# Kernel tuning notes

Hardware: AMD Instinct MI355X
Metric: run time of the kernel (lower is better)

The kernel has to match this reference:

```python
import jax, jax.numpy as jnp
import numpy as np

DEPTH = 2
DIM = 192
HEADS = 6
MLP_RATIO = 4

def _layernorm(x, g, b):
    mu = jnp.mean(x, -1, keepdims=True)
    var = jnp.var(x, -1, keepdims=True)
    return (x - mu) * jax.lax.rsqrt(var + 1e-5) * g + b

def _scanline_order(pos, w):
    # default space-filling curve of space_filling_cluster: horizontal scanlines
    # with alternating direction in each row (boustrophedon order)
    ix = jnp.floor(pos[..., 0]).astype(jnp.int32)
    iy = jnp.floor(pos[..., 1]).astype(jnp.int32)
    key = iy * w + jnp.where(iy % 2 == 1, w - 1 - ix, ix)
    order_idx = jnp.argsort(key, axis=1)      # rank -> token idx (b, n)
    inv_idx = jnp.argsort(order_idx, axis=1)  # token idx -> rank (b, n)
    return order_idx, inv_idx

def setup_inputs():
    key = jax.random.key(0)
    ks = jax.random.split(key, 8)
    b, h, w, m = 4, 128, 128, 64
    n = h * w
    d = DIM
    dff = MLP_RATIO * d
    s = 0.02
    x = jax.random.normal(ks[0], (b, n, d), jnp.float32)
    # token positions: the full h x w grid, randomly permuted per batch element
    ys, xs = jnp.meshgrid(jnp.arange(h), jnp.arange(w), indexing='ij')
    grid = jnp.stack([xs.reshape(-1), ys.reshape(-1)], -1).astype(jnp.float32)
    perm = jax.vmap(lambda kk: jax.random.permutation(kk, n))(jax.random.split(ks[1], b))
    pos = grid[perm]  # (b, n, 2)
    return {
        'x': x, 'pos': pos,
        'ln1_g': jnp.ones((DEPTH, d)), 'ln1_b': jnp.zeros((DEPTH, d)),
        'w_qkv': jax.random.normal(ks[2], (DEPTH, d, 3 * d), jnp.float32) * s,
        'b_qkv': jnp.zeros((DEPTH, 3 * d)),
        'w_proj': jax.random.normal(ks[3], (DEPTH, d, d), jnp.float32) * s,
        'b_proj': jnp.zeros((DEPTH, d)),
        'ln2_g': jnp.ones((DEPTH, d)), 'ln2_b': jnp.zeros((DEPTH, d)),
        'w_fc1': jax.random.normal(ks[4], (DEPTH, d, dff), jnp.float32) * s,
        'b_fc1': jnp.zeros((DEPTH, dff)),
        'w_fc2': jax.random.normal(ks[5], (DEPTH, dff, d), jnp.float32) * s,
        'b_fc2': jnp.zeros((DEPTH, d)),
        'h': h, 'w': w, 'm': m,
    }

def reference(x, pos, ln1_g, ln1_b, w_qkv, b_qkv, w_proj, b_proj,
              ln2_g, ln2_b, w_fc1, b_fc1, w_fc2, b_fc2, h, w, m):
    b, n, d = x.shape
    dh = d // HEADS
    scale = dh ** -0.5
    kc = n // m  # number of clusters (n chosen divisible by m -> all-ones cluster_mask)
    # clustering is computed under no_grad in the original -> stop_gradient
    order_idx, inv_idx = _scanline_order(jax.lax.stop_gradient(pos), w)
    for i in range(DEPTH):
        # --- cluster attention ---
        xn = _layernorm(x, ln1_g[i], ln1_b[i])
        qkv = xn @ w_qkv[i] + b_qkv[i]                                  # (b, n, 3d)
        qkv = jnp.take_along_axis(qkv, order_idx[..., None], axis=1)    # gather into curve order
        qkv = qkv.reshape(b, kc, m, 3, HEADS, dh)
        q = jnp.transpose(qkv[:, :, :, 0], (0, 1, 3, 2, 4))             # (b, kc, H, m, dh)
        kk = jnp.transpose(qkv[:, :, :, 1], (0, 1, 3, 2, 4))
        v = jnp.transpose(qkv[:, :, :, 2], (0, 1, 3, 2, 4))
        att = jax.nn.softmax(jnp.einsum('bkhqd,bkhpd->bkhqp', q, kk) * scale, axis=-1)
        o = jnp.einsum('bkhqp,bkhpd->bkhqd', att, v)
        o = jnp.transpose(o, (0, 1, 3, 2, 4)).reshape(b, n, d)
        o = jnp.take_along_axis(o, inv_idx[..., None], axis=1)          # scatter back to token order
        x = x + o @ w_proj[i] + b_proj[i]
        # --- MLP ---
        yn = _layernorm(x, ln2_g[i], ln2_b[i])
        x = x + jax.nn.gelu(yn @ w_fc1[i] + b_fc1[i]) @ w_fc2[i] + b_fc2[i]
    return x
```

## Files before the change

kernel.cpp:

```cpp
#include <hip/hip_runtime.h>
#include <hip/hip_bf16.h>

typedef __hip_bfloat16 bf16;
typedef __attribute__((ext_vector_type(8))) short short8;
typedef __attribute__((ext_vector_type(4))) short s16x4;
typedef __attribute__((ext_vector_type(4))) float f32x4;

#define B_   4
#define N_   16384
#define D_   192
#define H6   6
#define DH   32
#define MCL  64
#define KC   256
#define DFF  768
#define GW   128
#define MTOK (B_ * N_)
#define XST  196
#define PST  72
#define OST  40

__device__ __forceinline__ bf16 f2b(float x) { return __float2bfloat16(x); }
__device__ __forceinline__ short f2bbits(float x) {
    bf16 h = __float2bfloat16(x); return *(short*)&h;
}

__global__ void zero_out_kernel(float* __restrict__ out, size_t n) {
    size_t i = blockIdx.x * (size_t)blockDim.x + threadIdx.x;
    if (i < n) out[i] = 0.f;
}

__global__ void build_idx(const float* __restrict__ pos, int* __restrict__ order) {
    int tid = blockIdx.x * blockDim.x + threadIdx.x;
    if (tid >= B_ * N_) return;
    int b = tid / N_;
    int ix = (int)floorf(pos[(size_t)tid * 2 + 0]);
    int iy = (int)floorf(pos[(size_t)tid * 2 + 1]);
    int key = iy * GW + ((iy & 1) ? (GW - 1 - ix) : ix);
    key = (int)(((unsigned)key) & (N_ - 1));
    order[(size_t)b * N_ + key] = tid % N_;
}

__global__ void wprep_all(const float* __restrict__ wq, const float* __restrict__ wp,
                          const float* __restrict__ wf1, const float* __restrict__ wf2,
                          bf16* __restrict__ out) {
    int tid = blockIdx.x * blockDim.x + threadIdx.x;
    if (tid >= 2 * 442368) return;
    int l = tid / 442368, r = tid % 442368;
    const float* src; bf16* dst; int K, Nn, e;
    if (r < 110592)      { src = wq  + (size_t)l * 110592; dst = out + (size_t)l * 442368;          K = 192; Nn = 576; e = r; }
    else if (r < 147456) { src = wp  + (size_t)l * 36864;  dst = out + (size_t)l * 442368 + 110592; K = 192; Nn = 192; e = r - 110592; }
    else if (r < 294912) { src = wf1 + (size_t)l * 147456; dst = out + (size_t)l * 442368 + 147456; K = 192; Nn = 768; e = r - 147456; }
    else                 { src = wf2 + (size_t)l * 147456; dst = out + (size_t)l * 442368 + 294912; K = 768; Nn = 192; e = r - 294912; }
    int k = e / Nn, n = e % Nn;
    int idx = ((n >> 4) * (K >> 5) + (k >> 5)) * 512 + (((k >> 3) & 3) * 16 + (n & 15)) * 8 + (k & 7);
    dst[idx] = f2b(src[e]);
}

__global__ __launch_bounds__(384) void qa_fused(
    const float* __restrict__ xsrc, const int* __restrict__ order,
    const float* __restrict__ lng, const float* __restrict__ lnb,
    const bf16* __restrict__ Wqf, const float* __restrict__ bq,
    bf16* __restrict__ outb) {
    __shared__ short Asl[4 * 6 * 512];
    __shared__ short Qf[4 * 6 * 512];
    __shared__ short Kf[4 * 6 * 512];
    __shared__ short Vf[6 * 4 * 512];
    __shared__ short Pm[6 * 64 * PST];
    const float scale = 0.17677669529663687f;
    int c = blockIdx.x, b = blockIdx.y;
    int tid = threadIdx.x;
    int w = tid >> 6, lane = tid & 63;
    int quad = lane >> 4, l16 = lane & 15;
    int t = (int)(((unsigned)order[(size_t)b * N_ + c * MCL + lane]) & (N_ - 1));
    if (tid < 256) {
        int r = tid >> 2, qq = tid & 3;
        int tr = (int)(((unsigned)order[(size_t)b * N_ + c * MCL + r]) & (N_ - 1));
        const float* xr = xsrc + ((size_t)b * N_ + tr) * 192 + qq * 48;
        float4 va[12];
        float s = 0.f, ss = 0.f;
        #pragma unroll
        for (int j = 0; j < 12; j++) {
            va[j] = ((const float4*)xr)[j];
            s  += va[j].x + va[j].y + va[j].z + va[j].w;
            ss += va[j].x * va[j].x + va[j].y * va[j].y + va[j].z * va[j].z + va[j].w * va[j].w;
        }
        s  += __shfl_xor(s, 1);  s  += __shfl_xor(s, 2);
        ss += __shfl_xor(ss, 1); ss += __shfl_xor(ss, 2);
        float mean = s * (1.f / 192.f);
        float var  = ss * (1.f / 192.f) - mean * mean;
        float rs   = rsqrtf(var + 1e-5f);
        const float4* gg = (const float4*)(lng + qq * 48);
        const float4* bb = (const float4*)(lnb + qq * 48);
        #pragma unroll
        for (int j = 0; j < 6; j++) {
            float4 g0 = gg[2 * j], g1 = gg[2 * j + 1], b0 = bb[2 * j], b1v = bb[2 * j + 1];
            float4 x0 = va[2 * j], x1 = va[2 * j + 1];
            short8 o;
            o[0] = f2bbits((x0.x - mean) * rs * g0.x + b0.x);
            o[1] = f2bbits((x0.y - mean) * rs * g0.y + b0.y);
            o[2] = f2bbits((x0.z - mean) * rs * g0.z + b0.z);
            o[3] = f2bbits((x0.w - mean) * rs * g0.w + b0.w);
            o[4] = f2bbits((x1.x - mean) * rs * g1.x + b1v.x);
            o[5] = f2bbits((x1.y - mean) * rs * g1.y + b1v.y);
            o[6] = f2bbits((x1.z - mean) * rs * g1.z + b1v.z);
            o[7] = f2bbits((x1.w - mean) * rs * g1.w + b1v.w);
            int k0 = qq * 48 + j * 8;
            int kt = k0 >> 5, qd = (k0 >> 3) & 3;
            *(short8*)&Asl[((r >> 4) * 6 + kt) * 512 + (qd * 16 + (r & 15)) * 8] = o;
        }
    }
    __syncthreads();
    short8 af[4][6];
    #pragma unroll
    for (int mt = 0; mt < 4; mt++)
        #pragma unroll
        for (int kt = 0; kt < 6; kt++)
            af[mt][kt] = *(short8*)&Asl[(mt * 6 + kt) * 512 + lane * 8];
    #pragma unroll
    for (int s = 0; s < 4; s++) {
        int isK = s >> 1, q = s & 1;
        int nt = isK * 12 + 2 * w + q;
        const short* bp = (const short*)Wqf + ((size_t)nt * 6) * 512 + lane * 8;
        short8 bfr[6];
        #pragma unroll
        for (int kt = 0; kt < 6; kt++) bfr[kt] = *(const short8*)(bp + kt * 512);
        float4 bvq = *(const float4*)(bq + nt * 16 + quad * 4);
        short* dstb = isK ? Kf : Qf;
        #pragma unroll
        for (int mt = 0; mt < 4; mt++) {
            f32x4 a = {};
            #pragma unroll
            for (int kt = 0; kt < 6; kt++)
                a = __builtin_amdgcn_mfma_f32_16x16x32_bf16(bfr[kt], af[mt][kt], a, 0, 0, 0);
            s16x4 o;
            o[0] = f2bbits(a[0] + bvq.x); o[1] = f2bbits(a[1] + bvq.y);
            o[2] = f2bbits(a[2] + bvq.z); o[3] = f2bbits(a[3] + bvq.w);
            *(s16x4*)&dstb[(mt * 6 + w) * 512
                           + ((q * 2 + (quad >> 1)) * 16 + l16) * 8 + (quad & 1) * 4] = o;
        }
    }
    #pragma unroll
    for (int q = 0; q < 2; q++) {
        int nt = 24 + 2 * w + q;
        const short* bp = (const short*)Wqf + ((size_t)nt * 6) * 512 + lane * 8;
        short8 bfr[6];
        #pragma unroll
        for (int kt = 0; kt < 6; kt++) bfr[kt] = *(const short8*)(bp + kt * 512);
        float bvv = bq[nt * 16 + l16];
        #pragma unroll
        for (int mt = 0; mt < 4; mt++) {
            f32x4 a = {};
            #pragma unroll
            for (int kt = 0; kt < 6; kt++)
                a = __builtin_amdgcn_mfma_f32_16x16x32_bf16(af[mt][kt], bfr[kt], a, 0, 0, 0);
            s16x4 o;
            #pragma unroll
            for (int rr = 0; rr < 4; rr++) o[rr] = f2bbits(a[rr] + bvv);
            *(s16x4*)&Vf[((w * 2 + q) * 2 + (mt >> 1)) * 512
                         + (((mt & 1) * 2 + (quad >> 1)) * 16 + l16) * 8 + (quad & 1) * 4] = o;
        }
    }
    short8 aq[4], bk[4];
    #pragma unroll
    for (int i = 0; i < 4; i++) {
        aq[i] = *(short8*)&Qf[(i * 6 + w) * 512 + lane * 8];
        bk[i] = *(short8*)&Kf[(i * 6 + w) * 512 + lane * 8];
    }
    f32x4 S[4][4];
    #pragma unroll
    for (int mt = 0; mt < 4; mt++)
        #pragma unroll
        for (int nt = 0; nt < 4; nt++) {
            f32x4 z = {};
            S[mt][nt] = __builtin_amdgcn_mfma_f32_16x16x32_bf16(aq[mt], bk[nt], z, 0, 0, 0);
        }
    short* Pl = Pm + w * 64 * PST;
    #pragma unroll
    for (int mt = 0; mt < 4; mt++)
        #pragma unroll
        for (int r = 0; r < 4; r++) {
            float e0, e1, e2, e3, s;
            float v0 = S[mt][0][r] * scale, v1 = S[mt][1][r] * scale;
            float v2 = S[mt][2][r] * scale, v3 = S[mt][3][r] * scale;
            e0 = __expf(fminf(fmaxf(v0, -30.f), 30.f));
            e1 = __expf(fminf(fmaxf(v1, -30.f), 30.f));
            e2 = __expf(fminf(fmaxf(v2, -30.f), 30.f));
            e3 = __expf(fminf(fmaxf(v3, -30.f), 30.f));
            s = e0 + e1 + e2 + e3;
            s += __shfl_xor(s, 1); s += __shfl_xor(s, 2);
            s += __shfl_xor(s, 4); s += __shfl_xor(s, 8);
            float inv = 1.f / s;
            int row = mt * 16 + quad * 4 + r;
            Pl[row * PST +  0 + l16] = f2bbits(e0 * inv);
            Pl[row * PST + 16 + l16] = f2bbits(e1 * inv);
            Pl[row * PST + 32 + l16] = f2bbits(e2 * inv);
            Pl[row * PST + 48 + l16] = f2bbits(e3 * inv);
        }
    short8 ap[4][2], bv[2][2];
    #pragma unroll
    for (int mt = 0; mt < 4; mt++)
        #pragma unroll
        for (int kt = 0; kt < 2; kt++)
            ap[mt][kt] = *(const short8*)&Pl[(mt * 16 + l16) * PST + kt * 32 + quad * 8];
    #pragma unroll
    for (int nt = 0; nt < 2; nt++)
        #pragma unroll
        for (int kt = 0; kt < 2; kt++)
            bv[nt][kt] = *(const short8*)&Vf[((w * 2 + nt) * 2 + kt) * 512 + lane * 8];
    f32x4 O[4][2] = {};
    #pragma unroll
    for (int mt = 0; mt < 4; mt++)
        #pragma unroll
        for (int nt = 0; nt < 2; nt++)
            #pragma unroll
            for (int kt = 0; kt < 2; kt++)
                O[mt][nt] = __builtin_amdgcn_mfma_f32_16x16x32_bf16(ap[mt][kt], bv[nt][kt], O[mt][nt], 0, 0, 0);
    short* Ol = Pl;
    #pragma unroll
    for (int mt = 0; mt < 4; mt++) {
        int row = mt * 16 + quad * 4;
        #pragma unroll
        for (int nt = 0; nt < 2; nt++)
            #pragma unroll
            for (int rr = 0; rr < 4; rr++)
                Ol[(row + rr) * OST + nt * 16 + l16] = f2bbits(O[mt][nt][rr]);
    }
    short* op = (short*)outb + ((size_t)b * N_ + t) * 192 + w * 32;
    #pragma unroll
    for (int j = 0; j < 4; j++)
        *(short8*)(op + j * 8) = *(const short8*)&Ol[lane * OST + j * 8];
}

__global__ __launch_bounds__(256) void pm_fused(
    const bf16* __restrict__ Anob,
    const bf16* __restrict__ Wpf, const float* __restrict__ bp_,
    const float* __restrict__ Rsrc,
    const float* __restrict__ lng, const float* __restrict__ lnb,
    const bf16* __restrict__ W1f, const float* __restrict__ b1,
    const bf16* __restrict__ W2f, const float* __restrict__ b2,
    float* __restrict__ Rdst) {
    __shared__ float Xl[64 * XST];
    __shared__ short Bsl[4 * 6 * 512];
    short* Asl = (short*)Xl;
    int tid = threadIdx.x;
    int bm = blockIdx.x;
    int w = tid >> 6, lane = tid & 63;
    int quad = lane >> 4, l16 = lane & 15;
    {
        int r = tid >> 2, qq = tid & 3;
        const short* ar = (const short*)Anob + ((size_t)(bm * 64) + r) * 192 + qq * 48;
        #pragma unroll
        for (int j = 0; j < 6; j++) {
            short8 v = *(const short8*)(ar + j * 8);
            int k0 = qq * 48 + j * 8;
            int kt = k0 >> 5, qd = (k0 >> 3) & 3;
            *(short8*)&Asl[((r >> 4) * 6 + kt) * 512 + (qd * 16 + (r & 15)) * 8] = v;
        }
    }
    __syncthreads();
    short8 afp[6];
    #pragma unroll
    for (int kt = 0; kt < 6; kt++)
        afp[kt] = *(short8*)&Asl[(w * 6 + kt) * 512 + lane * 8];
    f32x4 acc[12];
    #pragma unroll
    for (int nt = 0; nt < 12; nt++) {
        const short* bp = (const short*)Wpf + ((size_t)nt * 6) * 512 + lane * 8;
        f32x4 a = {};
        #pragma unroll
        for (int kt = 0; kt < 6; kt++) {
            short8 b = *(const short8*)(bp + kt * 512);
            a = __builtin_amdgcn_mfma_f32_16x16x32_bf16(afp[kt], b, a, 0, 0, 0);
        }
        acc[nt] = a;
    }
    __syncthreads();
    #pragma unroll
    for (int nt = 0; nt < 12; nt++) {
        int col = nt * 16 + l16;
        float bv = bp_[col];
        int lr0 = w * 16 + quad * 4;
        #pragma unroll
        for (int rr = 0; rr < 4; rr++) {
            float rv = Rsrc[(size_t)(bm * 64 + lr0 + rr) * 192 + col];
            Xl[(lr0 + rr) * XST + col] = acc[nt][rr] + bv + rv;
        }
    }
    __syncthreads();
    {
        int r = tid >> 2, qq = tid & 3;
        const float* xr = &Xl[r * XST + qq * 48];
        float4 va[12];
        float s = 0.f, ss = 0.f;
        #pragma unroll
        for (int j = 0; j < 12; j++) {
            va[j] = ((const float4*)xr)[j];
            s  += va[j].x + va[j].y + va[j].z + va[j].w;
            ss += va[j].x * va[j].x + va[j].y * va[j].y + va[j].z * va[j].z + va[j].w * va[j].w;
        }
        s  += __shfl_xor(s, 1);  s  += __shfl_xor(s, 2);
        ss += __shfl_xor(ss, 1); ss += __shfl_xor(ss, 2);
        float mean = s * (1.f / 192.f);
        float var  = ss * (1.f / 192.f) - mean * mean;
        float rs   = rsqrtf(var + 1e-5f);
        const float4* gg = (const float4*)(lng + qq * 48);
        const float4* bb = (const float4*)(lnb + qq * 48);
        #pragma unroll
        for (int j = 0; j < 6; j++) {
            float4 g0 = gg[2 * j], g1 = gg[2 * j + 1], b0 = bb[2 * j], b1v = bb[2 * j + 1];
            float4 x0 = va[2 * j], x1 = va[2 * j + 1];
            short8 o;
            o[0] = f2bbits((x0.x - mean) * rs * g0.x + b0.x);
            o[1] = f2bbits((x0.y - mean) * rs * g0.y + b0.y);
            o[2] = f2bbits((x0.z - mean) * rs * g0.z + b0.z);
            o[3] = f2bbits((x0.w - mean) * rs * g0.w + b0.w);
            o[4] = f2bbits((x1.x - mean) * rs * g1.x + b1v.x);
            o[5] = f2bbits((x1.y - mean) * rs * g1.y + b1v.y);
            o[6] = f2bbits((x1.z - mean) * rs * g1.z + b1v.z);
            o[7] = f2bbits((x1.w - mean) * rs * g1.w + b1v.w);
            int k0 = qq * 48 + j * 8;
            int kt = k0 >> 5, qd = (k0 >> 3) & 3;
            *(short8*)&Bsl[((r >> 4) * 6 + kt) * 512 + (qd * 16 + (r & 15)) * 8] = o;
        }
    }
    __syncthreads();
    short8 af[4][6];
    #pragma unroll
    for (int mt = 0; mt < 4; mt++)
        #pragma unroll
        for (int kt = 0; kt < 6; kt++)
            af[mt][kt] = *(short8*)&Bsl[(mt * 6 + kt) * 512 + lane * 8];
    f32x4 acc2[3][4] = {};
    for (int qtr = 0; qtr < 4; qtr++) {
        __syncthreads();
        #pragma unroll
        for (int j = 0; j < 3; j++) {
            int nth = w * 3 + j;
            int ntg = qtr * 12 + nth;
            const short* bp = (const short*)W1f + ((size_t)ntg * 6) * 512 + lane * 8;
            short8 bfr[6];
            #pragma unroll
            for (int kt = 0; kt < 6; kt++) bfr[kt] = *(const short8*)(bp + kt * 512);
            #pragma unroll
            for (int mt = 0; mt < 4; mt++) {
                f32x4 a = {};
                #pragma unroll
                for (int kt = 0; kt < 6; kt++)
                    a = __builtin_amdgcn_mfma_f32_16x16x32_bf16(bfr[kt], af[mt][kt], a, 0, 0, 0);
                int colb = ntg * 16 + quad * 4;
                s16x4 o;
                #pragma unroll
                for (int rr = 0; rr < 4; rr++) {
                    float u = a[rr] + b1[colb + rr];
                    float inner = 0.7978845608028654f * (u + 0.044715f * u * u * u);
                    inner = fminf(fmaxf(inner, -12.f), 12.f);
                    float e = __expf(2.f * inner);
                    o[rr] = f2bbits(0.5f * u * (1.f + (e - 1.f) / (e + 1.f)));
                }
                *(s16x4*)&Bsl[(mt * 6 + (nth >> 1)) * 512
                              + (((nth & 1) * 2 + (quad >> 1)) * 16 + l16) * 8 + (quad & 1) * 4] = o;
            }
        }
        __syncthreads();
        #pragma unroll
        for (int kt = 0; kt < 6; kt++) {
            short8 afh[4];
            #pragma unroll
            for (int mt = 0; mt < 4; mt++)
                afh[mt] = *(short8*)&Bsl[(mt * 6 + kt) * 512 + lane * 8];
            #pragma unroll
            for (int j = 0; j < 3; j++) {
                int nt = w * 3 + j;
                const short* bp = (const short*)W2f + ((size_t)nt * 24 + qtr * 6 + kt) * 512 + lane * 8;
                short8 b = *(const short8*)bp;
                #pragma unroll
                for (int mt = 0; mt < 4; mt++)
                    acc2[j][mt] = __builtin_amdgcn_mfma_f32_16x16x32_bf16(afh[mt], b, acc2[j][mt], 0, 0, 0);
            }
        }
    }
    #pragma unroll
    for (int j = 0; j < 3; j++) {
        int col = (w * 3 + j) * 16 + l16;
        float bv = b2[col];
        #pragma unroll
        for (int mt = 0; mt < 4; mt++) {
            int lr0 = mt * 16 + quad * 4;
            #pragma unroll
            for (int rr = 0; rr < 4; rr++) {
                size_t idx = (size_t)(bm * 64 + lr0 + rr) * 192 + col;
                Rdst[idx] = acc2[j][mt][rr] + bv + Xl[(lr0 + rr) * XST + col];
            }
        }
    }
}

extern "C" void kernel_launch(void* const* d_in, const int* in_sizes, int n_in,
                              void* d_out, int out_size, void* d_ws, size_t ws_size,
                              hipStream_t stream) {
    const float* x_in   = (const float*)d_in[0];
    const float* pos    = (const float*)d_in[1];
    const float* ln1_g  = (const float*)d_in[2];
    const float* ln1_b  = (const float*)d_in[3];
    const float* w_qkv  = (const float*)d_in[4];
    const float* b_qkv  = (const float*)d_in[5];
    const float* w_proj = (const float*)d_in[6];
    const float* b_proj = (const float*)d_in[7];
    const float* ln2_g  = (const float*)d_in[8];
    const float* ln2_b  = (const float*)d_in[9];
    const float* w_fc1  = (const float*)d_in[10];
    const float* b_fc1  = (const float*)d_in[11];
    const float* w_fc2  = (const float*)d_in[12];
    const float* b_fc2  = (const float*)d_in[13];

    size_t sz_x     = (size_t)MTOK * D_ * 4;
    size_t sz_xnob  = (size_t)MTOK * D_ * 2;
    size_t sz_order = (size_t)B_ * N_ * 4;
    size_t sz_wbuf  = (size_t)2 * 442368 * 2;
    size_t need = sz_x + sz_xnob + sz_order + sz_wbuf;
    if (ws_size < need) {
        zero_out_kernel<<<(out_size + 255) / 256, 256, 0, stream>>>((float*)d_out, (size_t)out_size);
        return;
    }
    char* ws = (char*)d_ws;
    float* x_f32 = (float*)ws;  ws += sz_x;
    bf16*  xnob  = (bf16*)ws;   ws += sz_xnob;
    int*   order = (int*)ws;    ws += sz_order;
    bf16*  wbuf  = (bf16*)ws;   ws += sz_wbuf;

    bf16* wq[2]; bf16* wp[2]; bf16* wf1[2]; bf16* wf2[2];
    for (int l = 0; l < 2; ++l) {
        bf16* p = wbuf + (size_t)l * 442368;
        wq[l]  = p;
        wp[l]  = p + 110592;
        wf1[l] = p + 147456;
        wf2[l] = p + 294912;
    }
    wprep_all<<<(2 * 442368 + 255) / 256, 256, 0, stream>>>(w_qkv, w_proj, w_fc1, w_fc2, wbuf);
    build_idx<<<(B_ * N_ + 255) / 256, 256, 0, stream>>>(pos, order);

    for (int l = 0; l < 2; ++l) {
        const float* xsrc = (l == 0) ? x_in : x_f32;
        float* rdst = (l == 1) ? (float*)d_out : x_f32;
        qa_fused<<<dim3(KC, B_), 384, 0, stream>>>(
            xsrc, order, ln1_g + l * D_, ln1_b + l * D_,
            wq[l], b_qkv + l * 576, xnob);
        pm_fused<<<MTOK / 64, 256, 0, stream>>>(
            xnob, wp[l], b_proj + l * 192, xsrc,
            ln2_g + l * D_, ln2_b + l * D_,
            wf1[l], b_fc1 + l * 768, wf2[l], b_fc2 + l * 192,
            rdst);
    }
}
```

Before: 440.3 us.

## Fuse cluster attention, projection and MLP into one per-layer kernel

Merges the attention kernel and the projection+MLP kernel into a single kernel launched per cluster. The attention output now stays in shared memory and feeds the projection directly, removing the bf16 intermediate buffer's global write and read plus one launch per layer. The residual read and final output write now go to gathered, scattered token rows instead of contiguous rows. The MLP work is spread over six waves instead of four, and shared-memory regions are aliased across phases, which keeps LDS usage at about 150 KB per block.

```diff
diff --git a/kernel.cpp b/kernel.cpp
--- a/kernel.cpp
+++ b/kernel.cpp
@@ -18,7 +18,6 @@
 #define MTOK (B_ * N_)
 #define XST  196
 #define PST  72
-#define OST  40
 
 __device__ __forceinline__ bf16 f2b(float x) { return __float2bfloat16(x); }
 __device__ __forceinline__ short f2bbits(float x) {
@@ -57,16 +56,24 @@
     dst[idx] = f2b(src[e]);
 }
 
-__global__ __launch_bounds__(384) void qa_fused(
+__global__ __launch_bounds__(384) void layer_fused(
     const float* __restrict__ xsrc, const int* __restrict__ order,
-    const float* __restrict__ lng, const float* __restrict__ lnb,
+    const float* __restrict__ ln1g, const float* __restrict__ ln1b,
     const bf16* __restrict__ Wqf, const float* __restrict__ bq,
-    bf16* __restrict__ outb) {
-    __shared__ short Asl[4 * 6 * 512];
-    __shared__ short Qf[4 * 6 * 512];
-    __shared__ short Kf[4 * 6 * 512];
-    __shared__ short Vf[6 * 4 * 512];
-    __shared__ short Pm[6 * 64 * PST];
+    const bf16* __restrict__ Wpf, const float* __restrict__ bp_,
+    const float* __restrict__ ln2g, const float* __restrict__ ln2b,
+    const bf16* __restrict__ W1f, const float* __restrict__ b1,
+    const bf16* __restrict__ W2f, const float* __restrict__ b2,
+    float* __restrict__ Rdst) {
+    __shared__ __align__(16) char smem[153600];
+    short* Asl = (short*)smem;
+    short* Qf  = (short*)(smem + 24576);
+    short* Kf  = (short*)(smem + 49152);
+    short* Vf  = (short*)(smem + 73728);
+    short* Pm  = (short*)(smem + 98304);
+    float* Xl  = (float*)(smem + 98304);
+    short* Of  = Asl;
+    short* Bsl = Qf;
     const float scale = 0.17677669529663687f;
     int c = blockIdx.x, b = blockIdx.y;
     int tid = threadIdx.x;
@@ -90,8 +97,8 @@
         float mean = s * (1.f / 192.f);
         float var  = ss * (1.f / 192.f) - mean * mean;
         float rs   = rsqrtf(var + 1e-5f);
-        const float4* gg = (const float4*)(lng + qq * 48);
-        const float4* bb = (const float4*)(lnb + qq * 48);
+        const float4* gg = (const float4*)(ln1g + qq * 48);
+        const float4* bb = (const float4*)(ln1b + qq * 48);
         #pragma unroll
         for (int j = 0; j < 6; j++) {
             float4 g0 = gg[2 * j], g1 = gg[2 * j + 1], b0 = bb[2 * j], b1v = bb[2 * j + 1];
@@ -117,6 +124,7 @@
         #pragma unroll
         for (int kt = 0; kt < 6; kt++)
             af[mt][kt] = *(short8*)&Asl[(mt * 6 + kt) * 512 + lane * 8];
+    __syncthreads();
     #pragma unroll
     for (int s = 0; s < 4; s++) {
         int isK = s >> 1, q = s & 1;
@@ -161,134 +169,97 @@
                          + (((mt & 1) * 2 + (quad >> 1)) * 16 + l16) * 8 + (quad & 1) * 4] = o;
         }
     }
-    short8 aq[4], bk[4];
-    #pragma unroll
-    for (int i = 0; i < 4; i++) {
-        aq[i] = *(short8*)&Qf[(i * 6 + w) * 512 + lane * 8];
-        bk[i] = *(short8*)&Kf[(i * 6 + w) * 512 + lane * 8];
-    }
-    f32x4 S[4][4];
-    #pragma unroll
-    for (int mt = 0; mt < 4; mt++)
-        #pragma unroll
-        for (int nt = 0; nt < 4; nt++) {
-            f32x4 z = {};
-            S[mt][nt] = __builtin_amdgcn_mfma_f32_16x16x32_bf16(aq[mt], bk[nt], z, 0, 0, 0);
-        }
-    short* Pl = Pm + w * 64 * PST;
-    #pragma unroll
-    for (int mt = 0; mt < 4; mt++)
-        #pragma unroll
-        for (int r = 0; r < 4; r++) {
-            float e0, e1, e2, e3, s;
-            float v0 = S[mt][0][r] * scale, v1 = S[mt][1][r] * scale;
-            float v2 = S[mt][2][r] * scale, v3 = S[mt][3][r] * scale;
-            e0 = __expf(fminf(fmaxf(v0, -30.f), 30.f));
-            e1 = __expf(fminf(fmaxf(v1, -30.f), 30.f));
-            e2 = __expf(fminf(fmaxf(v2, -30.f), 30.f));
-            e3 = __expf(fminf(fmaxf(v3, -30.f), 30.f));
-            s = e0 + e1 + e2 + e3;
-            s += __shfl_xor(s, 1); s += __shfl_xor(s, 2);
-            s += __shfl_xor(s, 4); s += __shfl_xor(s, 8);
-            float inv = 1.f / s;
-            int row = mt * 16 + quad * 4 + r;
-            Pl[row * PST +  0 + l16] = f2bbits(e0 * inv);
-            Pl[row * PST + 16 + l16] = f2bbits(e1 * inv);
-            Pl[row * PST + 32 + l16] = f2bbits(e2 * inv);
-            Pl[row * PST + 48 + l16] = f2bbits(e3 * inv);
-        }
-    short8 ap[4][2], bv[2][2];
-    #pragma unroll
-    for (int mt = 0; mt < 4; mt++)
-        #pragma unroll
-        for (int kt = 0; kt < 2; kt++)
-            ap[mt][kt] = *(const short8*)&Pl[(mt * 16 + l16) * PST + kt * 32 + quad * 8];
-    #pragma unroll
-    for (int nt = 0; nt < 2; nt++)
-        #pragma unroll
-        for (int kt = 0; kt < 2; kt++)
-            bv[nt][kt] = *(const short8*)&Vf[((w * 2 + nt) * 2 + kt) * 512 + lane * 8];
-    f32x4 O[4][2] = {};
-    #pragma unroll
-    for (int mt = 0; mt < 4; mt++)
+    {
+        short8 aq[4], bk[4];
+        #pragma unroll
+        for (int i = 0; i < 4; i++) {
+            aq[i] = *(short8*)&Qf[(i * 6 + w) * 512 + lane * 8];
+            bk[i] = *(short8*)&Kf[(i * 6 + w) * 512 + lane * 8];
+        }
+        f32x4 S[4][4];
+        #pragma unroll
+        for (int mt = 0; mt < 4; mt++)
+            #pragma unroll
+            for (int nt = 0; nt < 4; nt++) {
+                f32x4 z = {};
+                S[mt][nt] = __builtin_amdgcn_mfma_f32_16x16x32_bf16(aq[mt], bk[nt], z, 0, 0, 0);
+            }
+        short* Pl = Pm + w * 64 * PST;
+        #pragma unroll
+        for (int mt = 0; mt < 4; mt++)
+            #pragma unroll
+            for (int r = 0; r < 4; r++) {
+                float e0, e1, e2, e3, s;
+                float v0 = S[mt][0][r] * scale, v1 = S[mt][1][r] * scale;
+                float v2 = S[mt][2][r] * scale, v3 = S[mt][3][r] * scale;
+                e0 = __expf(fminf(fmaxf(v0, -30.f), 30.f));
+                e1 = __expf(fminf(fmaxf(v1, -30.f), 30.f));
+                e2 = __expf(fminf(fmaxf(v2, -30.f), 30.f));
+                e3 = __expf(fminf(fmaxf(v3, -30.f), 30.f));
+                s = e0 + e1 + e2 + e3;
+                s += __shfl_xor(s, 1); s += __shfl_xor(s, 2);
+                s += __shfl_xor(s, 4); s += __shfl_xor(s, 8);
+                float inv = 1.f / s;
+                int row = mt * 16 + quad * 4 + r;
+                Pl[row * PST +  0 + l16] = f2bbits(e0 * inv);
+                Pl[row * PST + 16 + l16] = f2bbits(e1 * inv);
+                Pl[row * PST + 32 + l16] = f2bbits(e2 * inv);
+                Pl[row * PST + 48 + l16] = f2bbits(e3 * inv);
+            }
+        short8 ap[4][2], bv[2][2];
+        #pragma unroll
+        for (int mt = 0; mt < 4; mt++)
+            #pragma unroll
+            for (int kt = 0; kt < 2; kt++)
+                ap[mt][kt] = *(const short8*)&Pl[(mt * 16 + l16) * PST + kt * 32 + quad * 8];
         #pragma unroll
         for (int nt = 0; nt < 2; nt++)
             #pragma unroll
             for (int kt = 0; kt < 2; kt++)
-                O[mt][nt] = __builtin_amdgcn_mfma_f32_16x16x32_bf16(ap[mt][kt], bv[nt][kt], O[mt][nt], 0, 0, 0);
-    short* Ol = Pl;
-    #pragma unroll
-    for (int mt = 0; mt < 4; mt++) {
-        int row = mt * 16 + quad * 4;
-        #pragma unroll
-        for (int nt = 0; nt < 2; nt++)
-            #pragma unroll
-            for (int rr = 0; rr < 4; rr++)
-                Ol[(row + rr) * OST + nt * 16 + l16] = f2bbits(O[mt][nt][rr]);
-    }
-    short* op = (short*)outb + ((size_t)b * N_ + t) * 192 + w * 32;
-    #pragma unroll
-    for (int j = 0; j < 4; j++)
-        *(short8*)(op + j * 8) = *(const short8*)&Ol[lane * OST + j * 8];
-}
-
-__global__ __launch_bounds__(256) void pm_fused(
-    const bf16* __restrict__ Anob,
-    const bf16* __restrict__ Wpf, const float* __restrict__ bp_,
-    const float* __restrict__ Rsrc,
-    const float* __restrict__ lng, const float* __restrict__ lnb,
-    const bf16* __restrict__ W1f, const float* __restrict__ b1,
-    const bf16* __restrict__ W2f, const float* __restrict__ b2,
-    float* __restrict__ Rdst) {
-    __shared__ float Xl[64 * XST];
-    __shared__ short Bsl[4 * 6 * 512];
-    short* Asl = (short*)Xl;
-    int tid = threadIdx.x;
-    int bm = blockIdx.x;
-    int w = tid >> 6, lane = tid & 63;
-    int quad = lane >> 4, l16 = lane & 15;
-    {
-        int r = tid >> 2, qq = tid & 3;
-        const short* ar = (const short*)Anob + ((size_t)(bm * 64) + r) * 192 + qq * 48;
-        #pragma unroll
-        for (int j = 0; j < 6; j++) {
-            short8 v = *(const short8*)(ar + j * 8);
-            int k0 = qq * 48 + j * 8;
-            int kt = k0 >> 5, qd = (k0 >> 3) & 3;
-            *(short8*)&Asl[((r >> 4) * 6 + kt) * 512 + (qd * 16 + (r & 15)) * 8] = v;
-        }
+                bv[nt][kt] = *(const short8*)&Vf[((w * 2 + nt) * 2 + kt) * 512 + lane * 8];
+        #pragma unroll
+        for (int mt = 0; mt < 4; mt++)
+            #pragma unroll
+            for (int nt = 0; nt < 2; nt++) {
+                f32x4 ot = {};
+                #pragma unroll
+                for (int kt = 0; kt < 2; kt++)
+                    ot = __builtin_amdgcn_mfma_f32_16x16x32_bf16(bv[nt][kt], ap[mt][kt], ot, 0, 0, 0);
+                s16x4 o;
+                o[0] = f2bbits(ot[0]); o[1] = f2bbits(ot[1]);
+                o[2] = f2bbits(ot[2]); o[3] = f2bbits(ot[3]);
+                *(s16x4*)&Of[(mt * 6 + w) * 512
+                             + ((nt * 2 + (quad >> 1)) * 16 + l16) * 8 + (quad & 1) * 4] = o;
+            }
     }
     __syncthreads();
-    short8 afp[6];
-    #pragma unroll
-    for (int kt = 0; kt < 6; kt++)
-        afp[kt] = *(short8*)&Asl[(w * 6 + kt) * 512 + lane * 8];
-    f32x4 acc[12];
-    #pragma unroll
-    for (int nt = 0; nt < 12; nt++) {
-        const short* bp = (const short*)Wpf + ((size_t)nt * 6) * 512 + lane * 8;
-        f32x4 a = {};
-        #pragma unroll
-        for (int kt = 0; kt < 6; kt++) {
-            short8 b = *(const short8*)(bp + kt * 512);
-            a = __builtin_amdgcn_mfma_f32_16x16x32_bf16(afp[kt], b, a, 0, 0, 0);
-        }
-        acc[nt] = a;
+    if (w < 4) {
+        short8 afp[6];
+        #pragma unroll
+        for (int kt = 0; kt < 6; kt++)
+            afp[kt] = *(short8*)&Of[(w * 6 + kt) * 512 + lane * 8];
+        #pragma unroll
+        for (int nt = 0; nt < 12; nt++) {
+            const short* bp = (const short*)Wpf + ((size_t)nt * 6) * 512 + lane * 8;
+            f32x4 a = {};
+            #pragma unroll
+            for (int kt = 0; kt < 6; kt++) {
+                short8 bfr = *(const short8*)(bp + kt * 512);
+                a = __builtin_amdgcn_mfma_f32_16x16x32_bf16(afp[kt], bfr, a, 0, 0, 0);
+            }
+            int col = nt * 16 + l16;
+            float bv = bp_[col];
+            #pragma unroll
+            for (int rr = 0; rr < 4; rr++) {
+                int row = w * 16 + quad * 4 + rr;
+                int tr = __shfl(t, row);
+                float rv = xsrc[((size_t)b * N_ + tr) * 192 + col];
+                Xl[row * XST + col] = a[rr] + bv + rv;
+            }
+        }
     }
     __syncthreads();
-    #pragma unroll
-    for (int nt = 0; nt < 12; nt++) {
-        int col = nt * 16 + l16;
-        float bv = bp_[col];
-        int lr0 = w * 16 + quad * 4;
-        #pragma unroll
-        for (int rr = 0; rr < 4; rr++) {
-            float rv = Rsrc[(size_t)(bm * 64 + lr0 + rr) * 192 + col];
-            Xl[(lr0 + rr) * XST + col] = acc[nt][rr] + bv + rv;
-        }
-    }
-    __syncthreads();
-    {
+    if (tid < 256) {
         int r = tid >> 2, qq = tid & 3;
         const float* xr = &Xl[r * XST + qq * 48];
         float4 va[12];
@@ -304,8 +275,8 @@
         float mean = s * (1.f / 192.f);
         float var  = ss * (1.f / 192.f) - mean * mean;
         float rs   = rsqrtf(var + 1e-5f);
-        const float4* gg = (const float4*)(lng + qq * 48);
-        const float4* bb = (const float4*)(lnb + qq * 48);
+        const float4* gg = (const float4*)(ln2g + qq * 48);
+        const float4* bb = (const float4*)(ln2b + qq * 48);
         #pragma unroll
         for (int j = 0; j < 6; j++) {
             float4 g0 = gg[2 * j], g1 = gg[2 * j + 1], b0 = bb[2 * j], b1v = bb[2 * j + 1];
@@ -325,18 +296,18 @@
         }
     }
     __syncthreads();
-    short8 af[4][6];
+    short8 afm[4][6];
     #pragma unroll
     for (int mt = 0; mt < 4; mt++)
         #pragma unroll
         for (int kt = 0; kt < 6; kt++)
-            af[mt][kt] = *(short8*)&Bsl[(mt * 6 + kt) * 512 + lane * 8];
-    f32x4 acc2[3][4] = {};
+            afm[mt][kt] = *(short8*)&Bsl[(mt * 6 + kt) * 512 + lane * 8];
+    f32x4 acc2[2][4] = {};
     for (int qtr = 0; qtr < 4; qtr++) {
         __syncthreads();
         #pragma unroll
-        for (int j = 0; j < 3; j++) {
-            int nth = w * 3 + j;
+        for (int j = 0; j < 2; j++) {
+            int nth = w * 2 + j;
             int ntg = qtr * 12 + nth;
             const short* bp = (const short*)W1f + ((size_t)ntg * 6) * 512 + lane * 8;
             short8 bfr[6];
@@ -347,7 +318,7 @@
                 f32x4 a = {};
                 #pragma unroll
                 for (int kt = 0; kt < 6; kt++)
-                    a = __builtin_amdgcn_mfma_f32_16x16x32_bf16(bfr[kt], af[mt][kt], a, 0, 0, 0);
+                    a = __builtin_amdgcn_mfma_f32_16x16x32_bf16(bfr[kt], afm[mt][kt], a, 0, 0, 0);
                 int colb = ntg * 16 + quad * 4;
                 s16x4 o;
                 #pragma unroll
@@ -358,8 +329,8 @@
                     float e = __expf(2.f * inner);
                     o[rr] = f2bbits(0.5f * u * (1.f + (e - 1.f) / (e + 1.f)));
                 }
-                *(s16x4*)&Bsl[(mt * 6 + (nth >> 1)) * 512
-                              + (((nth & 1) * 2 + (quad >> 1)) * 16 + l16) * 8 + (quad & 1) * 4] = o;
+                *(s16x4*)&Bsl[(mt * 6 + w) * 512
+                              + ((j * 2 + (quad >> 1)) * 16 + l16) * 8 + (quad & 1) * 4] = o;
             }
         }
         __syncthreads();
@@ -370,27 +341,28 @@
             for (int mt = 0; mt < 4; mt++)
                 afh[mt] = *(short8*)&Bsl[(mt * 6 + kt) * 512 + lane * 8];
             #pragma unroll
-            for (int j = 0; j < 3; j++) {
-                int nt = w * 3 + j;
+            for (int j = 0; j < 2; j++) {
+                int nt = w * 2 + j;
                 const short* bp = (const short*)W2f + ((size_t)nt * 24 + qtr * 6 + kt) * 512 + lane * 8;
-                short8 b = *(const short8*)bp;
+                short8 bfr = *(const short8*)bp;
                 #pragma unroll
                 for (int mt = 0; mt < 4; mt++)
-                    acc2[j][mt] = __builtin_amdgcn_mfma_f32_16x16x32_bf16(afh[mt], b, acc2[j][mt], 0, 0, 0);
+                    acc2[j][mt] = __builtin_amdgcn_mfma_f32_16x16x32_bf16(afh[mt], bfr, acc2[j][mt], 0, 0, 0);
             }
         }
     }
     #pragma unroll
-    for (int j = 0; j < 3; j++) {
-        int col = (w * 3 + j) * 16 + l16;
+    for (int j = 0; j < 2; j++) {
+        int col = (w * 2 + j) * 16 + l16;
         float bv = b2[col];
         #pragma unroll
         for (int mt = 0; mt < 4; mt++) {
-            int lr0 = mt * 16 + quad * 4;
             #pragma unroll
             for (int rr = 0; rr < 4; rr++) {
-                size_t idx = (size_t)(bm * 64 + lr0 + rr) * 192 + col;
-                Rdst[idx] = acc2[j][mt][rr] + bv + Xl[(lr0 + rr) * XST + col];
+                int row = mt * 16 + quad * 4 + rr;
+                int tr = __shfl(t, row);
+                Rdst[((size_t)b * N_ + tr) * 192 + col] =
+                    acc2[j][mt][rr] + bv + Xl[row * XST + col];
             }
         }
     }
@@ -415,17 +387,15 @@
     const float* b_fc2  = (const float*)d_in[13];
 
     size_t sz_x     = (size_t)MTOK * D_ * 4;
-    size_t sz_xnob  = (size_t)MTOK * D_ * 2;
     size_t sz_order = (size_t)B_ * N_ * 4;
     size_t sz_wbuf  = (size_t)2 * 442368 * 2;
-    size_t need = sz_x + sz_xnob + sz_order + sz_wbuf;
+    size_t need = sz_x + sz_order + sz_wbuf;
     if (ws_size < need) {
         zero_out_kernel<<<(out_size + 255) / 256, 256, 0, stream>>>((float*)d_out, (size_t)out_size);
         return;
     }
     char* ws = (char*)d_ws;
     float* x_f32 = (float*)ws;  ws += sz_x;
-    bf16*  xnob  = (bf16*)ws;   ws += sz_xnob;
     int*   order = (int*)ws;    ws += sz_order;
     bf16*  wbuf  = (bf16*)ws;   ws += sz_wbuf;
 
@@ -443,11 +413,10 @@
     for (int l = 0; l < 2; ++l) {
         const float* xsrc = (l == 0) ? x_in : x_f32;
         float* rdst = (l == 1) ? (float*)d_out : x_f32;
-        qa_fused<<<dim3(KC, B_), 384, 0, stream>>>(
-            xsrc, order, ln1_g + l * D_, ln1_b + l * D_,
-            wq[l], b_qkv + l * 576, xnob);
-        pm_fused<<<MTOK / 64, 256, 0, stream>>>(
-            xnob, wp[l], b_proj + l * 192, xsrc,
+        layer_fused<<<dim3(KC, B_), 384, 0, stream>>>(
+            xsrc, order,
+            ln1_g + l * D_, ln1_b + l * D_, wq[l], b_qkv + l * 576,
+            wp[l], b_proj + l * 192,
             ln2_g + l * D_, ln2_b + l * D_,
             wf1[l], b_fc1 + l * 768, wf2[l], b_fc2 + l * 192,
             rdst);
```

After: 498.7 us. 1.13x slower.
